# Kernel tuning notes

Measured on AMD Instinct MI355X. Metric: run time of the kernel, lower is better.

## Reference

```python
import jax, jax.numpy as jnp
import numpy as np

EMB = 1024
HEADS = 16
HEAD_DIM = EMB // HEADS
DIM_FF = 4096
EPS = 1e-05


def layer_norm(x, gain, bias):
    # BasicLayerNorm: (x - mean) / (std + eps), std with unbiased=False
    mean = jnp.mean(x, axis=-1, keepdims=True)
    std = jnp.sqrt(jnp.mean((x - mean) ** 2, axis=-1, keepdims=True))
    return gain * ((x - mean) / (std + EPS)) + bias


def setup_inputs() -> dict:
    key = jax.random.key(0)
    ks = jax.random.split(key, 8)
    scale = 1.0 / np.sqrt(EMB)
    x = jax.random.normal(ks[0], (4, 2048, EMB), dtype=jnp.float32)
    Wq = jax.random.normal(ks[1], (EMB, EMB), dtype=jnp.float32) * scale
    Wk = jax.random.normal(ks[2], (EMB, EMB), dtype=jnp.float32) * scale
    Wv = jax.random.normal(ks[3], (EMB, EMB), dtype=jnp.float32) * scale
    Wo = jax.random.normal(ks[4], (EMB, EMB), dtype=jnp.float32) * scale
    W1 = jax.random.normal(ks[5], (EMB, DIM_FF), dtype=jnp.float32) * scale
    b1 = jnp.zeros((DIM_FF,), dtype=jnp.float32)
    W2 = jax.random.normal(ks[6], (DIM_FF, EMB), dtype=jnp.float32) * (1.0 / np.sqrt(DIM_FF))
    b2 = jnp.zeros((EMB,), dtype=jnp.float32)
    gain1 = jnp.ones((EMB,), dtype=jnp.float32)
    bias1 = jnp.zeros((EMB,), dtype=jnp.float32)
    gain2 = jnp.ones((EMB,), dtype=jnp.float32)
    bias2 = jnp.zeros((EMB,), dtype=jnp.float32)
    return dict(x=x, Wq=Wq, Wk=Wk, Wv=Wv, Wo=Wo, W1=W1, b1=b1, W2=W2, b2=b2,
                gain1=gain1, bias1=bias1, gain2=gain2, bias2=bias2)


def reference(x, Wq, Wk, Wv, Wo, W1, b1, W2, b2, gain1, bias1, gain2, bias2):
    b, t, e = x.shape
    h, dk = HEADS, HEAD_DIM
    # QKV projections, split heads -> (b, h, t, dk)
    q = (x @ Wq).reshape(b, t, h, dk).transpose(0, 2, 1, 3)
    k = (x @ Wk).reshape(b, t, h, dk).transpose(0, 2, 1, 3)
    v = (x @ Wv).reshape(b, t, h, dk).transpose(0, 2, 1, 3)
    # scaled dot-product attention
    scores = jnp.einsum('bhqd,bhkd->bhqk', q, k) / jnp.sqrt(jnp.float32(dk))
    attn = jax.nn.softmax(scores, axis=-1)
    ctx = jnp.einsum('bhqk,bhkd->bhqd', attn, v)
    # merge heads and output projection
    merged = ctx.transpose(0, 2, 1, 3).reshape(b, t, e)
    attended = merged @ Wo
    # residual + layer norm 1 (dropout is identity at inference)
    x1 = layer_norm(attended + x, gain1, bias1)
    # feed-forward
    ff = jax.nn.relu(x1 @ W1 + b1) @ W2 + b2
    # residual + layer norm 2
    return layer_norm(ff + x1, gain2, bias2)
```

## Files before the change

### kernel.cpp

```cpp
#include <hip/hip_runtime.h>
#include <hip/hip_bf16.h>
#include <math.h>

#define EMB 1024
#define DIM_FF 4096
#define HEADS 16
#define HD 64
#define TSEQ 2048
#define BATCH 4
#define MROWS (BATCH*TSEQ)
#define LN_EPS 1e-5f
#define QSCALE 0.18033688011f

typedef __attribute__((ext_vector_type(8))) short short8;
typedef __attribute__((ext_vector_type(4))) float f32x4;
typedef __attribute__((ext_vector_type(16))) float f32x16;

#define MFMA16(a,b,c) __builtin_amdgcn_mfma_f32_16x16x32_bf16((a),(b),(c),0,0,0)
#define MFMA32(a,b,c) __builtin_amdgcn_mfma_f32_32x32x16_bf16((a),(b),(c),0,0,0)

#define GLOBAL_AS(p) ((const __attribute__((address_space(1))) void*)(p))
#define LDS_AS(p)    ((__attribute__((address_space(3))) void*)(p))

__device__ __forceinline__ unsigned cvtpk_bf16(float lo, float hi){
    unsigned r;
    asm("v_cvt_pk_bf16_f32 %0, %1, %2" : "=v"(r) : "v"(lo), "v"(hi));
    return r;
}
__device__ __forceinline__ void permswap(unsigned &a, unsigned &b){
    asm("v_permlane32_swap_b32 %0, %1" : "+v"(a), "+v"(b));
}
__device__ __forceinline__ f32x4 ld4bf(const __hip_bfloat16* p){
    ushort4 u = *reinterpret_cast<const ushort4*>(p);
    union{unsigned i; float f;} c0,c1,c2,c3;
    c0.i=(unsigned)u.x<<16; c1.i=(unsigned)u.y<<16; c2.i=(unsigned)u.z<<16; c3.i=(unsigned)u.w<<16;
    f32x4 r; r[0]=c0.f; r[1]=c1.f; r[2]=c2.f; r[3]=c3.f;
    return r;
}
__device__ __forceinline__ int2 xcd_remap(){
    int bid = blockIdx.x + blockIdx.y * gridDim.x;
    int xcd = bid & 7, i = bid >> 3;
    int xpc = gridDim.x >> 3;
    int2 r;
    r.x = xcd * xpc + (i % xpc);
    r.y = i / xpc;
    return r;
}

__global__ __launch_bounds__(256)
void cvt_bf16(const float* __restrict__ in, __hip_bfloat16* __restrict__ out, int n4){
    int i = blockIdx.x*256 + threadIdx.x;
    if (i >= n4) return;
    f32x4 v = reinterpret_cast<const f32x4*>(in)[i];
    uint2 o;
    o.x = cvtpk_bf16(v[0], v[1]);
    o.y = cvtpk_bf16(v[2], v[3]);
    *reinterpret_cast<uint2*>(reinterpret_cast<unsigned short*>(out) + (size_t)i*4) = o;
}

__global__ __launch_bounds__(256)
void prep_weights(const float* __restrict__ Wq, const float* __restrict__ Wk,
                  const float* __restrict__ Wv, const float* __restrict__ Wo,
                  const float* __restrict__ W1, const float* __restrict__ W2,
                  __hip_bfloat16* __restrict__ Wqkv_t,
                  __hip_bfloat16* __restrict__ W1_t,
                  __hip_bfloat16* __restrict__ W2_t)
{
    const int id = blockIdx.x;
    const float* in; __hip_bfloat16* dst; int R, C, bx, by;
    if (id < 4096) {
        const int m = id >> 10, t = id & 1023;
        in  = m==0 ? Wq : m==1 ? Wk : m==2 ? Wv : Wo;
        dst = Wqkv_t + (size_t)m*1024*1024;
        R = 1024; C = 1024; bx = (t & 31)*32; by = (t >> 5)*32;
    } else if (id < 8192) {
        const int t = id - 4096;
        in = W1; dst = W1_t; R = 1024; C = 4096;
        bx = (t % 128)*32; by = (t / 128)*32;
    } else {
        const int t = id - 8192;
        in = W2; dst = W2_t; R = 4096; C = 1024;
        bx = (t % 32)*32; by = (t / 32)*32;
    }
    __shared__ __hip_bfloat16 tile[32][33];
    int x = bx + threadIdx.x;
    #pragma unroll
    for (int i = threadIdx.y; i < 32; i += 8)
        tile[i][threadIdx.x] = __float2bfloat16(in[(size_t)(by+i)*C + x]);
    __syncthreads();
    int xo = by + threadIdx.x;
    #pragma unroll
    for (int i = threadIdx.y; i < 32; i += 8)
        dst[(size_t)(bx+i)*R + xo] = tile[threadIdx.x][i];
}

template<int EPI>
__global__ __launch_bounds__(256, 4)
void gemm_bt(const __hip_bfloat16* __restrict__ A,
             const __hip_bfloat16* __restrict__ Bt,
             int M, int N, int K,
             __hip_bfloat16* __restrict__ Cb,
             const float* __restrict__ bias,
             __hip_bfloat16* __restrict__ qo,
             __hip_bfloat16* __restrict__ ko,
             __hip_bfloat16* __restrict__ vto)
{
    __shared__ __align__(16) __hip_bfloat16 As[128*32];
    __shared__ __align__(16) __hip_bfloat16 Bs[128*32];
    const int tid = threadIdx.x;
    const int lane = tid & 63;
    const int wid = tid >> 6;
    const int wm = wid >> 1, wn = wid & 1;
    const int2 bxy = xcd_remap();
    const int row0 = bxy.x * 128;
    const int col0 = bxy.y * 128;
    const int rA = lane & 15, kg = lane >> 4;
    const int csw = (rA >> 1) & 3;

    const int lrow = lane >> 2;
    const int lcol = ((lane & 3) ^ ((lane >> 3) & 3)) << 3;

    f32x4 acc[4][4] = {};

    for (int kt = 0; kt < K; kt += 32) {
        __syncthreads();
        #pragma unroll
        for (int half = 0; half < 2; ++half) {
            const int rbase = (wid << 5) + (half << 4);
            const int r = rbase + lrow;
            __builtin_amdgcn_global_load_lds(
                GLOBAL_AS(A + (size_t)(row0 + r)*K + kt + lcol),
                LDS_AS(&As[rbase*32]), 16, 0, 0);
            __builtin_amdgcn_global_load_lds(
                GLOBAL_AS(Bt + (size_t)(col0 + r)*K + kt + lcol),
                LDS_AS(&Bs[rbase*32]), 16, 0, 0);
        }
        __syncthreads();
        short8 af[4], bfr[4];
        #pragma unroll
        for (int mi = 0; mi < 4; ++mi)
            af[mi] = *reinterpret_cast<const short8*>(&As[(wm*64 + mi*16 + rA)*32 + ((kg ^ csw)<<3)]);
        #pragma unroll
        for (int ni = 0; ni < 4; ++ni)
            bfr[ni] = *reinterpret_cast<const short8*>(&Bs[(wn*64 + ni*16 + rA)*32 + ((kg ^ csw)<<3)]);
        #pragma unroll
        for (int mi = 0; mi < 4; ++mi)
            #pragma unroll
            for (int ni = 0; ni < 4; ++ni)
                acc[mi][ni] = MFMA16(af[mi], bfr[ni], acc[mi][ni]);
    }

    #pragma unroll
    for (int mi=0; mi<4; ++mi) {
        #pragma unroll
        for (int ni=0; ni<4; ++ni) {
            #pragma unroll
            for (int j=0;j<4;++j){
                float v = acc[mi][ni][j];
                int grow = row0 + wm*64 + mi*16 + (kg<<2) + j;
                int gcol = col0 + wn*64 + ni*16 + rA;
                if constexpr (EPI==0) {
                    int b = grow >> 11, t = grow & 2047;
                    int which = gcol >> 10, hdx = gcol & 1023;
                    int h = hdx >> 6, d = hdx & 63;
                    int bh = b*HEADS + h;
                    if (which==0)      qo[((size_t)bh*TSEQ + t)*HD + d] = __float2bfloat16(v*QSCALE);
                    else if (which==1) ko[((size_t)bh*TSEQ + t)*HD + d] = __float2bfloat16(v);
                    else               vto[((size_t)bh*HD + d)*TSEQ + t] = __float2bfloat16(v);
                } else if constexpr (EPI==2) {
                    v += bias[gcol]; v = v > 0.0f ? v : 0.0f;
                    Cb[(size_t)grow*N + gcol] = __float2bfloat16(v);
                } else {
                    if constexpr (EPI==3) v += bias[gcol];
                    Cb[(size_t)grow*N + gcol] = __float2bfloat16(v);
                }
            }
        }
    }
}

__global__ __launch_bounds__(256, 4)
void attn_fwd(const __hip_bfloat16* __restrict__ q,
              const __hip_bfloat16* __restrict__ k,
              const __hip_bfloat16* __restrict__ vt,
              __hip_bfloat16* __restrict__ merged)
{
    const int wg = (blockIdx.x & 7) * 128 + (blockIdx.x >> 3);
    const int bh = wg >> 4;
    const int qt = wg & 15;
    const int wid = threadIdx.x >> 6, lane = threadIdx.x & 63;
    const int l31 = lane & 31;
    const int hi  = lane >> 5;
    const int swz = lane & 7;
    const int qrow0 = qt*128 + wid*32;
    const __hip_bfloat16* Qh = q  + (size_t)bh*TSEQ*HD;
    const __hip_bfloat16* Kh = k  + (size_t)bh*TSEQ*HD;
    const __hip_bfloat16* Vh = vt + (size_t)bh*HD*TSEQ;

    __shared__ __align__(16) __hip_bfloat16 Kl[3][64*64];
    __shared__ __align__(16) __hip_bfloat16 Vl[2][64*64];

    short8 qv[4];
    #pragma unroll
    for (int c=0;c<4;++c)
        qv[c] = *reinterpret_cast<const short8*>(Qh + (size_t)(qrow0+l31)*HD + c*16 + hi*8);

    const int lrow = lane >> 3;
    const int lslot = ((lane & 7) ^ lrow) << 3;
    const __hip_bfloat16* sK0 = Kh + (size_t)(wid*16 + lrow)*HD + lslot;
    const __hip_bfloat16* sV0 = Vh + (size_t)(wid*16 + lrow)*TSEQ + lslot;
    const int dOff = wid*16*64;

    f32x16 O0 = {}, O1 = {};
    float lpart = 0.f;
    short8 paf[4] = {};

    auto stK = [&](int t){
        const int kt = t*64;
        __hip_bfloat16* dst = &Kl[t%3][dOff];
        __builtin_amdgcn_global_load_lds(GLOBAL_AS(sK0 + (size_t)kt*HD),     LDS_AS(dst),        16, 0, 0);
        __builtin_amdgcn_global_load_lds(GLOBAL_AS(sK0 + (size_t)(kt+8)*HD), LDS_AS(dst + 8*64), 16, 0, 0);
    };
    auto stV = [&](int t){
        __hip_bfloat16* dst = &Vl[t&1][dOff];
        __builtin_amdgcn_global_load_lds(GLOBAL_AS(sV0 + t*64),          LDS_AS(dst),        16, 0, 0);
        __builtin_amdgcn_global_load_lds(GLOBAL_AS(sV0 + 8*TSEQ + t*64), LDS_AS(dst + 8*64), 16, 0, 0);
    };

    const int NT = TSEQ/64;
    stK(0); stK(1);
    asm volatile("s_waitcnt vmcnt(2)" ::: "memory");
    __builtin_amdgcn_s_barrier();

    for (int t = 0; t < NT; ++t) {
        stV(t);
        if (t+2 < NT) stK(t+2);

        const char* Kb  = (const char*)&Kl[t%3][0];
        const char* Vbp = (const char*)&Vl[(t-1)&1][0];

        f32x16 st0 = {}, st1 = {};
        #pragma unroll
        for (int c=0;c<4;++c) {
            short8 ka0 = *reinterpret_cast<const short8*>(Kb + l31*128      + (((2*c+hi)^swz)<<4));
            short8 ka1 = *reinterpret_cast<const short8*>(Kb + (32+l31)*128 + (((2*c+hi)^swz)<<4));
            st0 = MFMA32(ka0, qv[c], st0);
            st1 = MFMA32(ka1, qv[c], st1);
        }

        if (t > 0) {
            #pragma unroll
            for (int kc=0; kc<4; ++kc) {
                short8 vf0 = *reinterpret_cast<const short8*>(Vbp + l31*128      + (((2*kc+hi)^swz)<<4));
                short8 vf1 = *reinterpret_cast<const short8*>(Vbp + (32+l31)*128 + (((2*kc+hi)^swz)<<4));
                O0 = MFMA32(paf[kc], vf0, O0);
                O1 = MFMA32(paf[kc], vf1, O1);
            }
        }

        #pragma unroll
        for (int r=0;r<16;++r) {
            st0[r] = __builtin_amdgcn_exp2f(st0[r]);
            st1[r] = __builtin_amdgcn_exp2f(st1[r]);
        }
        {
            f32x16 ss = st0 + st1;
            float s8 = (((ss[0]+ss[1])+(ss[2]+ss[3]))+((ss[4]+ss[5])+(ss[6]+ss[7])))
                     + (((ss[8]+ss[9])+(ss[10]+ss[11]))+((ss[12]+ss[13])+(ss[14]+ss[15])));
            lpart += s8;
        }
        unsigned pk0[8], pk1[8];
        #pragma unroll
        for (int j=0;j<8;++j) {
            pk0[j] = cvtpk_bf16(st0[2*j], st0[2*j+1]);
            pk1[j] = cvtpk_bf16(st1[2*j], st1[2*j+1]);
        }
        #pragma unroll
        for (int kc=0; kc<4; ++kc) {
            unsigned* pkt = (kc>>1) ? pk1 : pk0;
            const int j0 = 4*(kc&1);
            unsigned a0 = pkt[j0+0], b0 = pkt[j0+2];
            unsigned a1 = pkt[j0+1], b1 = pkt[j0+3];
            permswap(a0, b0);
            permswap(a1, b1);
            union { unsigned u[4]; short8 s; } pa;
            pa.u[0] = a0; pa.u[1] = a1; pa.u[2] = b0; pa.u[3] = b1;
            paf[kc] = pa.s;
        }

        if (t+2 < NT) { asm volatile("s_waitcnt vmcnt(2)" ::: "memory"); }
        else          { asm volatile("s_waitcnt vmcnt(0)" ::: "memory"); }
        __builtin_amdgcn_s_barrier();
    }
    {
        const char* Vbp = (const char*)&Vl[(NT-1)&1][0];
        #pragma unroll
        for (int kc=0; kc<4; ++kc) {
            short8 vf0 = *reinterpret_cast<const short8*>(Vbp + l31*128      + (((2*kc+hi)^swz)<<4));
            short8 vf1 = *reinterpret_cast<const short8*>(Vbp + (32+l31)*128 + (((2*kc+hi)^swz)<<4));
            O0 = MFMA32(paf[kc], vf0, O0);
            O1 = MFMA32(paf[kc], vf1, O1);
        }
    }

    lpart += __shfl_xor(lpart, 32);
    float linv = 1.0f / lpart;
    const int b = bh >> 4, h = bh & 15;
    #pragma unroll
    for (int r=0;r<16;++r){
        int qp = (r&3) + 8*(r>>2) + 4*hi;
        float lr = __shfl(linv, qp);
        size_t base = ((size_t)(b*TSEQ + qrow0 + qp))*EMB + h*HD;
        merged[base + l31]      = __float2bfloat16(O0[r]*lr);
        merged[base + 32 + l31] = __float2bfloat16(O1[r]*lr);
    }
}

template<int OUTF>
__global__ __launch_bounds__(256)
void ln_res_w(const __hip_bfloat16* __restrict__ a_, const __hip_bfloat16* __restrict__ res_,
              const float* __restrict__ gain, const float* __restrict__ bias,
              float* __restrict__ outf, __hip_bfloat16* __restrict__ outb)
{
    const int wave = threadIdx.x >> 6, lane = threadIdx.x & 63;
    const int row = blockIdx.x*4 + wave;
    const size_t base = (size_t)row * EMB;
    f32x4 v[4];
    float s = 0.f;
    #pragma unroll
    for (int j=0;j<4;++j){
        const int idx = j*256 + lane*4;
        f32x4 va = ld4bf(a_ + base + idx);
        f32x4 vr = ld4bf(res_ + base + idx);
        v[j] = va + vr;
        s += (v[j][0]+v[j][1]) + (v[j][2]+v[j][3]);
    }
    #pragma unroll
    for (int off=1; off<64; off<<=1) s += __shfl_xor(s, off);
    const float mean = s * (1.0f/EMB);
    float qs = 0.f;
    #pragma unroll
    for (int j=0;j<4;++j){
        #pragma unroll
        for (int e=0;e<4;++e){ float d = v[j][e] - mean; v[j][e] = d; qs += d*d; }
    }
    #pragma unroll
    for (int off=1; off<64; off<<=1) qs += __shfl_xor(qs, off);
    const float var = qs * (1.0f/EMB);
    const float r = 1.0f/(sqrtf(var)+LN_EPS);
    #pragma unroll
    for (int j=0;j<4;++j){
        const int idx = j*256 + lane*4;
        f32x4 g  = *reinterpret_cast<const f32x4*>(gain + idx);
        f32x4 bb = *reinterpret_cast<const f32x4*>(bias + idx);
        f32x4 o;
        #pragma unroll
        for (int e=0;e<4;++e) o[e] = g[e]*(v[j][e]*r) + bb[e];
        if constexpr (OUTF) {
            *reinterpret_cast<f32x4*>(outf + base + idx) = o;
        } else {
            uint2 ob;
            ob.x = cvtpk_bf16(o[0], o[1]);
            ob.y = cvtpk_bf16(o[2], o[3]);
            *reinterpret_cast<uint2*>(reinterpret_cast<unsigned short*>(outb) + base + idx) = ob;
        }
    }
}

extern "C" void kernel_launch(void* const* d_in, const int* in_sizes, int n_in,
                              void* d_out, int out_size, void* d_ws, size_t ws_size,
                              hipStream_t stream) {
    const float* x   = (const float*)d_in[0];
    const float* Wq  = (const float*)d_in[1];
    const float* Wk  = (const float*)d_in[2];
    const float* Wv  = (const float*)d_in[3];
    const float* Wo  = (const float*)d_in[4];
    const float* W1  = (const float*)d_in[5];
    const float* b1  = (const float*)d_in[6];
    const float* W2  = (const float*)d_in[7];
    const float* b2  = (const float*)d_in[8];
    const float* gain1 = (const float*)d_in[9];
    const float* bias1 = (const float*)d_in[10];
    const float* gain2 = (const float*)d_in[11];
    const float* bias2 = (const float*)d_in[12];

    char* ws = (char*)d_ws;
    __hip_bfloat16* Wqkv_t   = (__hip_bfloat16*)(ws + 0);
    __hip_bfloat16* Wo_t     = (__hip_bfloat16*)(ws + 6291456);
    __hip_bfloat16* W1_t     = (__hip_bfloat16*)(ws + 8388608);
    __hip_bfloat16* W2_t     = (__hip_bfloat16*)(ws + 16777216);
    __hip_bfloat16* xb       = (__hip_bfloat16*)(ws + 25165824);
    __hip_bfloat16* qb       = (__hip_bfloat16*)(ws + 41943040);
    __hip_bfloat16* kbuf     = (__hip_bfloat16*)(ws + 58720256);
    __hip_bfloat16* vtb      = (__hip_bfloat16*)(ws + 75497472);
    __hip_bfloat16* h1       = (__hip_bfloat16*)(ws + 25165824);
    __hip_bfloat16* mergedb  = (__hip_bfloat16*)(ws + 92274688);
    __hip_bfloat16* ffb      = (__hip_bfloat16*)(ws + 92274688);
    __hip_bfloat16* attendedb= (__hip_bfloat16*)(ws + 109051904);
    __hip_bfloat16* x1b      = (__hip_bfloat16*)(ws + 125829120);
    float*          outf     = (float*)d_out;

    prep_weights<<<dim3(12288), dim3(32,8), 0, stream>>>(Wq, Wk, Wv, Wo, W1, W2,
                                                         Wqkv_t, W1_t, W2_t);
    cvt_bf16<<<(MROWS*EMB/4 + 255)/256, 256, 0, stream>>>(x, xb, MROWS*EMB/4);

    gemm_bt<0><<<dim3(MROWS/128, 3072/128), 256, 0, stream>>>(
        xb, Wqkv_t, MROWS, 3072, EMB, nullptr, nullptr, qb, kbuf, vtb);
    attn_fwd<<<dim3(1024), 256, 0, stream>>>(qb, kbuf, vtb, mergedb);
    gemm_bt<1><<<dim3(MROWS/128, EMB/128), 256, 0, stream>>>(
        mergedb, Wo_t, MROWS, EMB, EMB, attendedb, nullptr, nullptr, nullptr, nullptr);
    ln_res_w<0><<<MROWS/4, 256, 0, stream>>>(attendedb, xb, gain1, bias1, nullptr, x1b);
    gemm_bt<2><<<dim3(MROWS/128, DIM_FF/128), 256, 0, stream>>>(
        x1b, W1_t, MROWS, DIM_FF, EMB, h1, b1, nullptr, nullptr, nullptr);
    gemm_bt<3><<<dim3(MROWS/128, EMB/128), 256, 0, stream>>>(
        h1, W2_t, MROWS, EMB, DIM_FF, ffb, b2, nullptr, nullptr, nullptr);
    ln_res_w<1><<<MROWS/4, 256, 0, stream>>>(ffb, x1b, gain2, bias2, outf, nullptr);
}
```

Before: 393.2 us.

## Use 256x256 tile GEMM with 16 waves for QKV and FF1 projections

```diff
diff --git a/kernel.cpp b/kernel.cpp
--- a/kernel.cpp
+++ b/kernel.cpp
@@ -100,10 +100,7 @@
              const __hip_bfloat16* __restrict__ Bt,
              int M, int N, int K,
              __hip_bfloat16* __restrict__ Cb,
-             const float* __restrict__ bias,
-             __hip_bfloat16* __restrict__ qo,
-             __hip_bfloat16* __restrict__ ko,
-             __hip_bfloat16* __restrict__ vto)
+             const float* __restrict__ bias)
 {
     __shared__ __align__(16) __hip_bfloat16 As[128*32];
     __shared__ __align__(16) __hip_bfloat16 Bs[128*32];
@@ -127,6 +124,77 @@
         #pragma unroll
         for (int half = 0; half < 2; ++half) {
             const int rbase = (wid << 5) + (half << 4);
+            const int r = rbase + lrow;
+            __builtin_amdgcn_global_load_lds(
+                GLOBAL_AS(A + (size_t)(row0 + r)*K + kt + lcol),
+                LDS_AS(&As[rbase*32]), 16, 0, 0);
+            __builtin_amdgcn_global_load_lds(
+                GLOBAL_AS(Bt + (size_t)(col0 + r)*K + kt + lcol),
+                LDS_AS(&Bs[rbase*32]), 16, 0, 0);
+        }
+        __syncthreads();
+        short8 af[4], bfr[4];
+        #pragma unroll
+        for (int mi = 0; mi < 4; ++mi)
+            af[mi] = *reinterpret_cast<const short8*>(&As[(wm*64 + mi*16 + rA)*32 + ((kg ^ csw)<<3)]);
+        #pragma unroll
+        for (int ni = 0; ni < 4; ++ni)
+            bfr[ni] = *reinterpret_cast<const short8*>(&Bs[(wn*64 + ni*16 + rA)*32 + ((kg ^ csw)<<3)]);
+        #pragma unroll
+        for (int mi = 0; mi < 4; ++mi)
+            #pragma unroll
+            for (int ni = 0; ni < 4; ++ni)
+                acc[mi][ni] = MFMA16(af[mi], bfr[ni], acc[mi][ni]);
+    }
+
+    #pragma unroll
+    for (int mi=0; mi<4; ++mi) {
+        #pragma unroll
+        for (int ni=0; ni<4; ++ni) {
+            #pragma unroll
+            for (int j=0;j<4;++j){
+                float v = acc[mi][ni][j];
+                int grow = row0 + wm*64 + mi*16 + (kg<<2) + j;
+                int gcol = col0 + wn*64 + ni*16 + rA;
+                if constexpr (EPI==3) v += bias[gcol];
+                Cb[(size_t)grow*N + gcol] = __float2bfloat16(v);
+            }
+        }
+    }
+}
+
+template<int EPI>
+__global__ __launch_bounds__(1024, 2)
+void gemm256s(const __hip_bfloat16* __restrict__ A,
+              const __hip_bfloat16* __restrict__ Bt,
+              int M, int N, int K,
+              __hip_bfloat16* __restrict__ Cb,
+              const float* __restrict__ bias,
+              __hip_bfloat16* __restrict__ qo,
+              __hip_bfloat16* __restrict__ ko,
+              __hip_bfloat16* __restrict__ vto)
+{
+    __shared__ __align__(16) __hip_bfloat16 As[256*32];
+    __shared__ __align__(16) __hip_bfloat16 Bs[256*32];
+    const int tid = threadIdx.x;
+    const int lane = tid & 63;
+    const int wid = tid >> 6;
+    const int wm = wid >> 2, wn = wid & 3;
+    const int2 bxy = xcd_remap();
+    const int row0 = bxy.x * 256;
+    const int col0 = bxy.y * 256;
+    const int rA = lane & 15, kg = lane >> 4;
+    const int csw = (rA >> 1) & 3;
+
+    const int lrow = lane >> 2;
+    const int lcol = ((lane & 3) ^ ((lane >> 3) & 3)) << 3;
+
+    f32x4 acc[4][4] = {};
+
+    for (int kt = 0; kt < K; kt += 32) {
+        __syncthreads();
+        {
+            const int rbase = wid << 4;
             const int r = rbase + lrow;
             __builtin_amdgcn_global_load_lds(
                 GLOBAL_AS(A + (size_t)(row0 + r)*K + kt + lcol),
@@ -167,11 +235,8 @@
                     if (which==0)      qo[((size_t)bh*TSEQ + t)*HD + d] = __float2bfloat16(v*QSCALE);
                     else if (which==1) ko[((size_t)bh*TSEQ + t)*HD + d] = __float2bfloat16(v);
                     else               vto[((size_t)bh*HD + d)*TSEQ + t] = __float2bfloat16(v);
-                } else if constexpr (EPI==2) {
+                } else {
                     v += bias[gcol]; v = v > 0.0f ? v : 0.0f;
-                    Cb[(size_t)grow*N + gcol] = __float2bfloat16(v);
-                } else {
-                    if constexpr (EPI==3) v += bias[gcol];
                     Cb[(size_t)grow*N + gcol] = __float2bfloat16(v);
                 }
             }
@@ -404,15 +469,15 @@
                                                          Wqkv_t, W1_t, W2_t);
     cvt_bf16<<<(MROWS*EMB/4 + 255)/256, 256, 0, stream>>>(x, xb, MROWS*EMB/4);
 
-    gemm_bt<0><<<dim3(MROWS/128, 3072/128), 256, 0, stream>>>(
+    gemm256s<0><<<dim3(MROWS/256, 3072/256), 1024, 0, stream>>>(
         xb, Wqkv_t, MROWS, 3072, EMB, nullptr, nullptr, qb, kbuf, vtb);
     attn_fwd<<<dim3(1024), 256, 0, stream>>>(qb, kbuf, vtb, mergedb);
     gemm_bt<1><<<dim3(MROWS/128, EMB/128), 256, 0, stream>>>(
-        mergedb, Wo_t, MROWS, EMB, EMB, attendedb, nullptr, nullptr, nullptr, nullptr);
+        mergedb, Wo_t, MROWS, EMB, EMB, attendedb, nullptr);
     ln_res_w<0><<<MROWS/4, 256, 0, stream>>>(attendedb, xb, gain1, bias1, nullptr, x1b);
-    gemm_bt<2><<<dim3(MROWS/128, DIM_FF/128), 256, 0, stream>>>(
+    gemm256s<2><<<dim3(MROWS/256, DIM_FF/256), 1024, 0, stream>>>(
         x1b, W1_t, MROWS, DIM_FF, EMB, h1, b1, nullptr, nullptr, nullptr);
     gemm_bt<3><<<dim3(MROWS/128, EMB/128), 256, 0, stream>>>(
-        h1, W2_t, MROWS, EMB, DIM_FF, ffb, b2, nullptr, nullptr, nullptr);
+        h1, W2_t, MROWS, EMB, DIM_FF, ffb, b2);
     ln_res_w<1><<<MROWS/4, 256, 0, stream>>>(ffb, x1b, gain2, bias2, outf, nullptr);
 }
```

After: 432.0 us. 1.1x slower.
